# Performance work log

Hardware: AMD Instinct MI355X
Metric: run time of the kernel (lower is better)

The kernel has to match this reference:

```python
import jax, jax.numpy as jnp
import numpy as np

NUM_OBJ = 3
MIN_OBJ_SCALE = 0.1
MAX_OBJ_SCALE = 0.8
MIN_Y_SCALE = 0.75
MAX_Y_SCALE = 1.25
OBJ_POS_BOUND = 0.9
EPS_FIX = 0.095
BIG = 1e12


def setup_inputs() -> dict:
    key = jax.random.key(0)
    k1, k2, k3 = jax.random.split(key, 3)
    n, T, C, H, W = 64, 32, 3, 64, 64
    x = jax.random.normal(k1, (n, T, C, H, W), dtype=jnp.float32)
    d = C * H * W
    W_enc = jax.random.normal(k2, (d, NUM_OBJ * 8), dtype=jnp.float32) / np.sqrt(d).astype(np.float32)
    b_enc = jax.random.normal(k3, (NUM_OBJ * 8,), dtype=jnp.float32) * 0.01
    return {"x": x, "W_enc": W_enc, "b_enc": b_enc}


def _constrain_zp_mean(zp):
    # zp: (nTo, 8) -> mean (nTo, 4). std branch is discarded by forward().
    zm = jnp.concatenate([jax.nn.sigmoid(zp[:, 0:2]), 2.0 * jax.nn.sigmoid(zp[:, 2:4]) - 1.0], -1)
    set_max = jnp.array([[MAX_OBJ_SCALE - MIN_OBJ_SCALE, MAX_Y_SCALE - MIN_Y_SCALE, OBJ_POS_BOUND, OBJ_POS_BOUND]], dtype=zp.dtype)
    set_min = jnp.array([[MIN_OBJ_SCALE, MIN_Y_SCALE, 0.0, 0.0]], dtype=zp.dtype)
    return zm * set_max + set_min


def _greedy_assign(errors):
    # errors: (n, o, o). Greedy row-by-row argmin, masking out used columns with BIG,
    # exactly as the torch fault-fix loop does via scatter of 1e12.
    n, o, _ = errors.shape
    def step(used, i):
        e = errors[:, i, :] + used * BIG
        j = jnp.argmin(e, -1)
        used = used + jax.nn.one_hot(j, o, dtype=errors.dtype)
        return used, j
    _, js = jax.lax.scan(step, jnp.zeros((n, o), errors.dtype), jnp.arange(o))
    return jnp.moveaxis(js, 0, 1)  # (n, o)


def _match_objects(z):
    # z: (n, T, o, 4). Sequential greedy matching over time.
    def step(prev, z_t):
        curr = jax.lax.stop_gradient(z_t[:, :, 2:4])          # (n, o, 2)
        prv = jax.lax.stop_gradient(prev[:, :, 2:4])          # (n, o, 2)
        errors = jnp.sum((prv[:, :, None, :] - curr[:, None, :, :]) ** 2, -1)  # (n, i, j)
        idx = jnp.argmin(errors, -1)                          # (n, o)
        # fault = assignment is not a permutation (num_obj==3 check from source)
        ok = jnp.all(idx[:, 1:] != idx[:, :-1], -1) & (idx[:, 0] != idx[:, 2])
        gidx = _greedy_assign(errors)
        idx = jnp.where(ok[:, None], idx, gidx)
        match = jnp.take_along_axis(z_t, idx[:, :, None], axis=1)
        return match, match
    z0 = z[:, 0]
    _, rest = jax.lax.scan(step, z0, jnp.moveaxis(z[:, 1:], 1, 0))
    return jnp.concatenate([z0[:, None], jnp.moveaxis(rest, 0, 1)], 1)


def _fix_supair(z):
    # z: (n, T, o, 4). Replace isolated position jumps with neighbor average.
    n, T, o, d = z.shape
    diffs = jax.lax.stop_gradient(jnp.abs(z[:, 1:, :, :2] - z[:, :-1, :, :2]))
    zpad2 = jnp.zeros((n, 1, o, 2), z.dtype)
    prev = jnp.concatenate([zpad2, diffs], 1)
    after = jnp.concatenate([diffs, zpad2], 1)
    mask = (prev > EPS_FIX) & (after > EPS_FIX)               # (n, T, o, 2)
    zpad = jnp.zeros((n, 1, o, d), z.dtype)
    smooth = jnp.concatenate([zpad, (z[:, :-2] + z[:, 2:]) / 2, zpad], 1)
    mask_full = jnp.concatenate((d // 2) * [mask], -1)        # (n, T, o, 4)
    return jnp.where(mask_full, smooth, z)


def reference(x, W_enc, b_enc):
    n, T = x.shape[0], x.shape[1]
    # encoder: per-frame linear to (num_obj, 8) z-parameters
    zp = x.reshape(n * T, -1) @ W_enc + b_enc                  # (nT, o*8)
    zm = _constrain_zp_mean(zp.reshape(-1, 8))                 # (nTo, 4)
    z = zm.reshape(n, T, NUM_OBJ, 4)
    z = _match_objects(z)
    z = _fix_supair(z)
    # v_from_state
    v = z[:, 1:, :, 2:] - z[:, :-1, :, 2:]
    zf = jnp.concatenate([z[:, 1:], v], -1)                    # (n, T-1, o, 6)
    zf = jnp.concatenate([jnp.zeros_like(zf[:, 0:1]), zf], 1)  # (n, T, o, 6)
    zf = zf[:, 1:, :, 2:]                                      # (n, T-1, o, 4)
    zf = jnp.concatenate([(zf[..., :2] + 1) / 2 * 10, zf[..., 2:] / 2 * 10], -1)
    zf = jnp.concatenate([zf[..., :2] / 5, zf[..., 2:] * 2], -1)
    return zf
```

## Files before the change

### kernel.cpp

```cpp
#include <hip/hip_runtime.h>

#define N_B   64
#define T_S   32
#define DIM   12288
#define ROWS  2048
#define NCOL  12
#define RPW   4
#define WAVES 4
#define RPB   (RPW * WAVES)
#define KSPL  16
#define KSEG  (DIM / KSPL)
#define JSTEP (KSEG / 256)

__global__ __launch_bounds__(256) void k_gemm(const float* __restrict__ x,
                                              const float* __restrict__ W,
                                              float* __restrict__ part) {
    __shared__ float wt[NCOL * KSEG];
    const int rb   = blockIdx.x >> 4;
    const int sg   = blockIdx.x & 15;
    const int tid  = threadIdx.x;
    const int wave = tid >> 6;
    const int lane = tid & 63;
    const int r0   = rb * RPB + wave * RPW;
    const int k00  = sg * KSEG;

#pragma unroll
    for (int it = 0; it < 9; ++it) {
        const int flat = tid + it * 256;
        const int k    = flat / 3;
        const int g    = flat - 3 * k;
        const float4 wv = *(const float4*)(W + (size_t)(k00 + k) * 24 + g * 8);
        float* d = wt + (g * 4) * KSEG + k;
        d[0 * KSEG] = wv.x;
        d[1 * KSEG] = wv.y;
        d[2 * KSEG] = wv.z;
        d[3 * KSEG] = wv.w;
    }

    float4 xv[JSTEP][RPW];
#pragma unroll
    for (int j = 0; j < JSTEP; ++j)
#pragma unroll
        for (int r = 0; r < RPW; ++r)
            xv[j][r] = *(const float4*)(x + (size_t)(r0 + r) * DIM + k00 + j * 256 + lane * 4);

    __syncthreads();

    float acc[RPW][NCOL];
#pragma unroll
    for (int r = 0; r < RPW; ++r)
#pragma unroll
        for (int c = 0; c < NCOL; ++c) acc[r][c] = 0.f;

#pragma unroll
    for (int j = 0; j < JSTEP; ++j) {
        const int kl = j * 256 + lane * 4;
#pragma unroll
        for (int c = 0; c < NCOL; ++c) {
            const float4 wv = *(const float4*)(wt + c * KSEG + kl);
#pragma unroll
            for (int r = 0; r < RPW; ++r)
                acc[r][c] += xv[j][r].x * wv.x + xv[j][r].y * wv.y +
                             xv[j][r].z * wv.z + xv[j][r].w * wv.w;
        }
    }

#pragma unroll
    for (int r = 0; r < RPW; ++r)
#pragma unroll
        for (int c = 0; c < NCOL; ++c) {
            float v = acc[r][c];
            v += __shfl_xor(v, 32, 64);
            v += __shfl_xor(v, 16, 64);
            v += __shfl_xor(v, 8, 64);
            v += __shfl_xor(v, 4, 64);
            v += __shfl_xor(v, 2, 64);
            v += __shfl_xor(v, 1, 64);
            acc[r][c] = v;
        }

    __syncthreads();
    float* red = wt;
    if (lane == 0) {
#pragma unroll
        for (int r = 0; r < RPW; ++r)
#pragma unroll
            for (int c = 0; c < NCOL; ++c)
                red[(wave * RPW + r) * NCOL + c] = acc[r][c];
    }
    __syncthreads();

    if (tid < RPB * NCOL)
        part[(size_t)sg * (ROWS * NCOL) + (size_t)rb * (RPB * NCOL) + tid] = red[tid];
}

__global__ __launch_bounds__(256) void k_reduce(const float* __restrict__ part,
                                                const float* __restrict__ b_enc,
                                                float* __restrict__ zbuf) {
    const int rc = blockIdx.x * 256 + threadIdx.x;
    float s = 0.f;
#pragma unroll
    for (int i = 0; i < KSPL; ++i) s += part[(size_t)i * (ROWS * NCOL) + rc];

    const int row = rc / NCOL;
    const int c   = rc - row * NCOL;
    const int o   = c >> 2;
    const int cp  = c & 3;
    s += b_enc[o * 8 + cp];
    const float sg = 1.f / (1.f + expf(-s));
    float v;
    if (cp == 0)      v = sg * 0.7f + 0.1f;
    else if (cp == 1) v = sg * 0.5f + 0.75f;
    else              v = (2.f * sg - 1.f) * 0.9f;
    zbuf[rc] = v;
}

__global__ __launch_bounds__(64) void k_post(const float* __restrict__ zbuf,
                                             float* __restrict__ out) {
    __shared__ float z[T_S * NCOL];
    __shared__ float zm[T_S * NCOL];
    __shared__ float zf[T_S * NCOL];
    __shared__ int   perm[T_S];
    const int b   = blockIdx.x;
    const int tid = threadIdx.x;

#pragma unroll
    for (int i = 0; i < 6; ++i)
        z[tid + 64 * i] = zbuf[b * 384 + tid + 64 * i];
    __syncthreads();

    if (tid == 0) {
        float px0 = z[2],  py0 = z[3];
        float px1 = z[6],  py1 = z[7];
        float px2 = z[10], py2 = z[11];
        for (int t = 1; t < T_S; ++t) {
            const int base = t * 12;
            const float cx0 = z[base + 2],  cy0 = z[base + 3];
            const float cx1 = z[base + 6],  cy1 = z[base + 7];
            const float cx2 = z[base + 10], cy2 = z[base + 11];

            float dx, dy;
            dx = px0 - cx0; dy = py0 - cy0; const float e00 = dx * dx + dy * dy;
            dx = px0 - cx1; dy = py0 - cy1; const float e01 = dx * dx + dy * dy;
            dx = px0 - cx2; dy = py0 - cy2; const float e02 = dx * dx + dy * dy;
            dx = px1 - cx0; dy = py1 - cy0; const float e10 = dx * dx + dy * dy;
            dx = px1 - cx1; dy = py1 - cy1; const float e11 = dx * dx + dy * dy;
            dx = px1 - cx2; dy = py1 - cy2; const float e12 = dx * dx + dy * dy;
            dx = px2 - cx0; dy = py2 - cy0; const float e20 = dx * dx + dy * dy;
            dx = px2 - cx1; dy = py2 - cy1; const float e21 = dx * dx + dy * dy;
            dx = px2 - cx2; dy = py2 - cy2; const float e22 = dx * dx + dy * dy;

            auto amin3 = [](float a0, float a1, float a2) {
                int j = 0; float e = a0;
                if (a1 < e) { e = a1; j = 1; }
                if (a2 < e) { j = 2; }
                return j;
            };
            int i0 = amin3(e00, e01, e02);
            int i1 = amin3(e10, e11, e12);
            int i2 = amin3(e20, e21, e22);
            const bool ok = (i1 != i0) && (i2 != i1) && (i0 != i2);
            if (!ok) {
                float u0 = 0.f, u1 = 0.f, u2 = 0.f;
                i0 = amin3(e00, e01, e02);
                if (i0 == 0) u0 = 1.f; else if (i0 == 1) u1 = 1.f; else u2 = 1.f;
                i1 = amin3(e10 + u0 * 1e12f, e11 + u1 * 1e12f, e12 + u2 * 1e12f);
                if (i1 == 0) u0 = 1.f; else if (i1 == 1) u1 = 1.f; else u2 = 1.f;
                i2 = amin3(e20 + u0 * 1e12f, e21 + u1 * 1e12f, e22 + u2 * 1e12f);
            }
            perm[t] = i0 * 9 + i1 * 3 + i2;
            px0 = (i0 == 0) ? cx0 : (i0 == 1) ? cx1 : cx2;
            py0 = (i0 == 0) ? cy0 : (i0 == 1) ? cy1 : cy2;
            px1 = (i1 == 0) ? cx0 : (i1 == 1) ? cx1 : cx2;
            py1 = (i1 == 0) ? cy0 : (i1 == 1) ? cy1 : cy2;
            px2 = (i2 == 0) ? cx0 : (i2 == 1) ? cx1 : cx2;
            py2 = (i2 == 0) ? cy0 : (i2 == 1) ? cy1 : cy2;
        }
    }
    __syncthreads();

#pragma unroll
    for (int ii = 0; ii < 6; ++ii) {
        const int i  = tid + 64 * ii;
        const int t  = i / 12;
        const int j  = i - t * 12;
        const int k  = j >> 2;
        const int ch = j & 3;
        int p = k;
        if (t > 0) {
            const int code = perm[t];
            p = (k == 0) ? code / 9 : (k == 1) ? (code % 9) / 3 : code % 3;
        }
        zm[i] = z[t * 12 + p * 4 + ch];
    }
    __syncthreads();

#pragma unroll
    for (int ii = 0; ii < 6; ++ii) {
        const int i  = tid + 64 * ii;
        const int t  = i / 12;
        const int j  = i - t * 12;
        const int o  = j >> 2;
        const int cc = j & 1;
        const int mb = o * 4 + cc;
        const float pd = (t >= 1)  ? fabsf(zm[t * 12 + mb] - zm[(t - 1) * 12 + mb]) : 0.f;
        const float ad = (t <= 30) ? fabsf(zm[(t + 1) * 12 + mb] - zm[t * 12 + mb]) : 0.f;
        const bool  m  = (pd > 0.095f) && (ad > 0.095f);
        const float sm = (t >= 1 && t <= 30)
                             ? (zm[(t - 1) * 12 + j] + zm[(t + 1) * 12 + j]) * 0.5f
                             : 0.f;
        zf[i] = m ? sm : zm[t * 12 + j];
    }
    __syncthreads();

    for (int i = tid; i < 31 * 12; i += 64) {
        const int t  = i / 12;
        const int j  = i - t * 12;
        const int o  = j >> 2;
        const int c2 = j & 3;
        const int pb = o * 4 + 2 + (c2 & 1);
        float v;
        if (c2 < 2) v = zf[(t + 1) * 12 + pb] + 1.f;
        else        v = (zf[(t + 1) * 12 + pb] - zf[t * 12 + pb]) * 10.f;
        out[b * 372 + i] = v;
    }
}

extern "C" void kernel_launch(void* const* d_in, const int* in_sizes, int n_in,
                              void* d_out, int out_size, void* d_ws, size_t ws_size,
                              hipStream_t stream) {
    (void)in_sizes; (void)n_in; (void)out_size; (void)ws_size;
    const float* x     = (const float*)d_in[0];
    const float* W_enc = (const float*)d_in[1];
    const float* b_enc = (const float*)d_in[2];
    float* out  = (float*)d_out;

    float* zbuf = (float*)d_ws;
    float* part = zbuf + ROWS * NCOL;

    k_gemm  <<<(ROWS / RPB) * KSPL, 256, 0, stream>>>(x, W_enc, part);
    k_reduce<<<(ROWS * NCOL) / 256, 256, 0, stream>>>(part, b_enc, zbuf);
    k_post  <<<N_B, 64, 0, stream>>>(zbuf, out);
}
```

Measured before the change: 170.3 us.

## Restructure GEMM to stage x tiles in LDS and use wave-uniform W loads

The GEMM kernel now copies a 64-row by 128-column tile of x into padded shared memory, and each lane accumulates all 12 outputs for its own row. Each wave reads its slice of W_enc through wave-uniform addresses, which replaces the per-thread W transpose and the large cross-lane shuffle reduction. The K dimension is split into many more segments (96 instead of 16). That enlarges the partial-sum buffer and the work in the reduce kernel, and it needs more workspace memory.

```diff
diff --git a/kernel.cpp b/kernel.cpp
--- a/kernel.cpp
+++ b/kernel.cpp
@@ -5,93 +5,79 @@
 #define DIM   12288
 #define ROWS  2048
 #define NCOL  12
-#define RPW   4
-#define WAVES 4
-#define RPB   (RPW * WAVES)
-#define KSPL  16
-#define KSEG  (DIM / KSPL)
-#define JSTEP (KSEG / 256)
+#define RPBK  64
+#define KB    128
+#define KSPL  (DIM / KB)
+#define XSTR  133
+
+typedef float f4 __attribute__((ext_vector_type(4)));
 
 __global__ __launch_bounds__(256) void k_gemm(const float* __restrict__ x,
                                               const float* __restrict__ W,
                                               float* __restrict__ part) {
-    __shared__ float wt[NCOL * KSEG];
-    const int rb   = blockIdx.x >> 4;
-    const int sg   = blockIdx.x & 15;
-    const int tid  = threadIdx.x;
-    const int wave = tid >> 6;
+    __shared__ float xs[RPBK * XSTR];
+    const int bx  = blockIdx.x;
+    const int rg  = bx / KSPL;
+    const int sg  = bx - rg * KSPL;
+    const int tid = threadIdx.x;
+    const int r0  = rg * RPBK;
+    const int kb0 = sg * KB;
+
+#pragma unroll
+    for (int it = 0; it < 8; ++it) {
+        const int flat = tid + it * 256;
+        const int row  = flat >> 5;
+        const int c4   = flat & 31;
+        const f4 v = *(const f4*)(x + (size_t)(r0 + row) * DIM + kb0 + c4 * 4);
+        *(f4*)(xs + row * XSTR + c4 * 4) = v;
+    }
+    __syncthreads();
+
+    const int w    = __builtin_amdgcn_readfirstlane(tid >> 6);
     const int lane = tid & 63;
-    const int r0   = rb * RPB + wave * RPW;
-    const int k00  = sg * KSEG;
-
-#pragma unroll
-    for (int it = 0; it < 9; ++it) {
-        const int flat = tid + it * 256;
-        const int k    = flat / 3;
-        const int g    = flat - 3 * k;
-        const float4 wv = *(const float4*)(W + (size_t)(k00 + k) * 24 + g * 8);
-        float* d = wt + (g * 4) * KSEG + k;
-        d[0 * KSEG] = wv.x;
-        d[1 * KSEG] = wv.y;
-        d[2 * KSEG] = wv.z;
-        d[3 * KSEG] = wv.w;
-    }
-
-    float4 xv[JSTEP][RPW];
-#pragma unroll
-    for (int j = 0; j < JSTEP; ++j)
-#pragma unroll
-        for (int r = 0; r < RPW; ++r)
-            xv[j][r] = *(const float4*)(x + (size_t)(r0 + r) * DIM + k00 + j * 256 + lane * 4);
-
-    __syncthreads();
-
-    float acc[RPW][NCOL];
-#pragma unroll
-    for (int r = 0; r < RPW; ++r)
-#pragma unroll
-        for (int c = 0; c < NCOL; ++c) acc[r][c] = 0.f;
-
-#pragma unroll
-    for (int j = 0; j < JSTEP; ++j) {
-        const int kl = j * 256 + lane * 4;
-#pragma unroll
-        for (int c = 0; c < NCOL; ++c) {
-            const float4 wv = *(const float4*)(wt + c * KSEG + kl);
-#pragma unroll
-            for (int r = 0; r < RPW; ++r)
-                acc[r][c] += xv[j][r].x * wv.x + xv[j][r].y * wv.y +
-                             xv[j][r].z * wv.z + xv[j][r].w * wv.w;
+
+    f4 xr[8];
+#pragma unroll
+    for (int i = 0; i < 8; ++i)
+        xr[i] = *(const f4*)(xs + lane * XSTR + w * 32 + i * 4);
+
+    float acc[NCOL];
+#pragma unroll
+    for (int c = 0; c < NCOL; ++c) acc[c] = 0.f;
+
+    const float* wbase = W + (size_t)(kb0 + w * 32) * 24;
+#pragma unroll
+    for (int i = 0; i < 8; ++i) {
+#pragma unroll
+        for (int kk = 0; kk < 4; ++kk) {
+            const float  xv = xr[i][kk];
+            const float* wr = wbase + (i * 4 + kk) * 24;
+            acc[0]  += xv * wr[0];  acc[1]  += xv * wr[1];
+            acc[2]  += xv * wr[2];  acc[3]  += xv * wr[3];
+            acc[4]  += xv * wr[8];  acc[5]  += xv * wr[9];
+            acc[6]  += xv * wr[10]; acc[7]  += xv * wr[11];
+            acc[8]  += xv * wr[16]; acc[9]  += xv * wr[17];
+            acc[10] += xv * wr[18]; acc[11] += xv * wr[19];
         }
     }
-
-#pragma unroll
-    for (int r = 0; r < RPW; ++r)
-#pragma unroll
-        for (int c = 0; c < NCOL; ++c) {
-            float v = acc[r][c];
-            v += __shfl_xor(v, 32, 64);
-            v += __shfl_xor(v, 16, 64);
-            v += __shfl_xor(v, 8, 64);
-            v += __shfl_xor(v, 4, 64);
-            v += __shfl_xor(v, 2, 64);
-            v += __shfl_xor(v, 1, 64);
-            acc[r][c] = v;
-        }
-
-    __syncthreads();
-    float* red = wt;
-    if (lane == 0) {
-#pragma unroll
-        for (int r = 0; r < RPW; ++r)
-#pragma unroll
-            for (int c = 0; c < NCOL; ++c)
-                red[(wave * RPW + r) * NCOL + c] = acc[r][c];
-    }
-    __syncthreads();
-
-    if (tid < RPB * NCOL)
-        part[(size_t)sg * (ROWS * NCOL) + (size_t)rb * (RPB * NCOL) + tid] = red[tid];
+    __syncthreads();
+
+#pragma unroll
+    for (int c = 0; c < NCOL; ++c)
+        xs[w * (64 * 13) + lane * 13 + c] = acc[c];
+    __syncthreads();
+
+#pragma unroll
+    for (int j = 0; j < 3; ++j) {
+        const int i   = tid + j * 256;
+        const int row = i / NCOL;
+        const int c   = i - row * NCOL;
+        float s = 0.f;
+#pragma unroll
+        for (int ww = 0; ww < 4; ++ww)
+            s += xs[ww * (64 * 13) + row * 13 + c];
+        part[(size_t)sg * (ROWS * NCOL) + (size_t)rg * (RPBK * NCOL) + i] = s;
+    }
 }
 
 __global__ __launch_bounds__(256) void k_reduce(const float* __restrict__ part,
@@ -99,7 +85,7 @@
                                                 float* __restrict__ zbuf) {
     const int rc = blockIdx.x * 256 + threadIdx.x;
     float s = 0.f;
-#pragma unroll
+#pragma unroll 8
     for (int i = 0; i < KSPL; ++i) s += part[(size_t)i * (ROWS * NCOL) + rc];
 
     const int row = rc / NCOL;
@@ -238,7 +224,7 @@
     float* zbuf = (float*)d_ws;
     float* part = zbuf + ROWS * NCOL;
 
-    k_gemm  <<<(ROWS / RPB) * KSPL, 256, 0, stream>>>(x, W_enc, part);
+    k_gemm  <<<(ROWS / RPBK) * KSPL, 256, 0, stream>>>(x, W_enc, part);
     k_reduce<<<(ROWS * NCOL) / 256, 256, 0, stream>>>(part, b_enc, zbuf);
     k_post  <<<N_B, 64, 0, stream>>>(zbuf, out);
 }
```

New measurement: 176.6 us. +3.7%, slower.
